# Kernel optimization log

Measured on AMD Instinct MI355X. Metric: run time of the kernel, lower is better.

The kernel has to match this reference:

```python
import jax, jax.numpy as jnp
import numpy as np

B, S, H, F, E, TOP_K = 2, 2048, 1024, 2048, 8, 2


def setup_inputs() -> dict:
    key = jax.random.key(0)
    ks = jax.random.split(key, 5)
    scale_h = 1.0 / np.sqrt(H)
    scale_f = 1.0 / np.sqrt(F)
    return {
        "hidden_states": jax.random.normal(ks[0], (B, S, H), jnp.float32),
        "gate_w": jax.random.normal(ks[1], (H, E), jnp.float32) * scale_h,
        "w_up": jax.random.normal(ks[2], (E, H, F), jnp.float32) * scale_h,
        "w_gate": jax.random.normal(ks[3], (E, H, F), jnp.float32) * scale_h,
        "w_down": jax.random.normal(ks[4], (E, F, H), jnp.float32) * scale_f,
    }


def reference(hidden_states, gate_w, w_up, w_gate, w_down):
    b, s, h = hidden_states.shape
    x = hidden_states.reshape(-1, h)                      # [T, H]
    T = x.shape[0]

    # Router: softmax then top-k then renormalize (as in the module)
    router_logits = x @ gate_w                            # [T, E]
    probs = jax.nn.softmax(router_logits, axis=-1)
    routing_weights, selected_experts = jax.lax.top_k(probs, TOP_K)  # [T, K]
    routing_weights = routing_weights / jnp.sum(routing_weights, axis=-1, keepdims=True)
    routing_weights = routing_weights.astype(x.dtype)

    # Per-token combine weight for each expert (sum over k where selected == e).
    # Equals the masked where/+ accumulation in the original (zero where unselected).
    combine = jnp.zeros((T, E), x.dtype).at[
        jnp.arange(T)[:, None], selected_experts
    ].add(routing_weights)                                # [T, E]

    # Dense expert compute on ALL tokens for every expert (faithful to original,
    # where each device runs its expert on the full token set, then psum).
    up = jnp.einsum("th,ehf->etf", x, w_up)               # [E, T, F]
    gate = jnp.einsum("th,ehf->etf", x, w_gate)           # [E, T, F]
    inner = jax.nn.silu(up) * gate                        # note: silu on up_proj, as in source
    expert_out = jnp.einsum("etf,efh->eth", inner, w_down)  # [E, T, H]

    # Weighted combine == psum over expert axis of masked/weighted outputs.
    y = jnp.einsum("te,eth->th", combine, expert_out)     # [T, H]
    return y.reshape(b, s, h)
```

## Files before the change

### kernel.cpp

```cpp
#include <hip/hip_runtime.h>
#include <hip/hip_bf16.h>

typedef __bf16 bf16x8 __attribute__((ext_vector_type(8)));
typedef float f32x4 __attribute__((ext_vector_type(4)));

#define T_TOK 4096
#define H_DIM 1024
#define F_DIM 2048
#define NEXP 8
#define TOTROWS 8192
#define MAXTILES 80

__device__ inline unsigned short f2b(float f) {
    unsigned int u = __float_as_uint(f);
    unsigned int r = (u + 0x7fffu + ((u >> 16) & 1u)) >> 16;
    return (unsigned short)r;
}

__global__ __launch_bounds__(256) void router_kernel(const float* __restrict__ x,
                                                     const float* __restrict__ gw,
                                                     int* __restrict__ sel, float* __restrict__ selw) {
    int t = blockIdx.x * 4 + (threadIdx.x >> 6);
    int lane = threadIdx.x & 63;
    float acc[8] = {0.f,0.f,0.f,0.f,0.f,0.f,0.f,0.f};
    const float* xr = x + (size_t)t * H_DIM;
    for (int h = lane; h < H_DIM; h += 64) {
        float xv = xr[h];
        const float4* g = (const float4*)(gw + h * 8);
        float4 g0 = g[0], g1 = g[1];
        acc[0] += xv * g0.x; acc[1] += xv * g0.y; acc[2] += xv * g0.z; acc[3] += xv * g0.w;
        acc[4] += xv * g1.x; acc[5] += xv * g1.y; acc[6] += xv * g1.z; acc[7] += xv * g1.w;
    }
#pragma unroll
    for (int off = 32; off >= 1; off >>= 1)
#pragma unroll
        for (int e = 0; e < 8; ++e)
            acc[e] += __shfl_down(acc[e], off);
    if (lane == 0) {
        float mx = acc[0];
#pragma unroll
        for (int e = 1; e < 8; ++e) mx = fmaxf(mx, acc[e]);
        float p[8]; float s = 0.f;
#pragma unroll
        for (int e = 0; e < 8; ++e) { p[e] = expf(acc[e] - mx); s += p[e]; }
        float inv_s = 1.f / s;
#pragma unroll
        for (int e = 0; e < 8; ++e) p[e] *= inv_s;
        int e1 = 0; float p1 = p[0];
#pragma unroll
        for (int e = 1; e < 8; ++e) if (p[e] > p1) { p1 = p[e]; e1 = e; }
        int e2 = -1; float p2 = -1.f;
#pragma unroll
        for (int e = 0; e < 8; ++e) { if (e == e1) continue; if (p[e] > p2) { p2 = p[e]; e2 = e; } }
        float inv = 1.f / (p1 + p2);
        sel[t * 2 + 0] = e1; sel[t * 2 + 1] = e2;
        selw[t * 2 + 0] = p1 * inv; selw[t * 2 + 1] = p2 * inv;
    }
}

__global__ __launch_bounds__(256) void scan_kernel(const int* __restrict__ sel,
                                                   int* __restrict__ cnt, int* __restrict__ off,
                                                   int* __restrict__ fill,
                                                   int* __restrict__ tileExp, int* __restrict__ tileM0) {
    __shared__ int h[NEXP];
    int tid = threadIdx.x;
    if (tid < NEXP) h[tid] = 0;
    __syncthreads();
    for (int i = tid; i < TOTROWS; i += 256) atomicAdd(&h[sel[i]], 1);
    __syncthreads();
    if (tid == 0) {
        int o = 0;
        for (int e = 0; e < NEXP; ++e) { cnt[e] = h[e]; off[e] = o; o += h[e]; fill[e] = 0; }
        int nt = 0;
        for (int e = 0; e < NEXP; ++e)
            for (int m0 = 0; m0 < h[e]; m0 += 128) { tileExp[nt] = e; tileM0[nt] = m0; nt++; }
        for (int i = nt; i < MAXTILES; ++i) { tileExp[i] = -1; tileM0[i] = 0; }
    }
}

__global__ __launch_bounds__(256) void scatgath_kernel(const int* __restrict__ sel,
                                                       const float* __restrict__ selw,
                                                       const int* __restrict__ off,
                                                       int* __restrict__ fill,
                                                       float* __restrict__ rowWgt,
                                                       int* __restrict__ tokRow,
                                                       const float* __restrict__ x,
                                                       unsigned short* __restrict__ Xg) {
    __shared__ int rs[2];
    int t = blockIdx.x;
    int tid = threadIdx.x;
    if (tid == 0) {
#pragma unroll
        for (int k = 0; k < 2; ++k) {
            int e = sel[t * 2 + k];
            int slot = atomicAdd(&fill[e], 1);
            int r = off[e] + slot;
            rowWgt[r] = selw[t * 2 + k];
            tokRow[t * 2 + k] = r;
            rs[k] = r;
        }
    }
    __syncthreads();
    int r1 = rs[0], r2 = rs[1];
    float4 v = ((const float4*)(x + (size_t)t * H_DIM))[tid];
    ushort4 o;
    o.x = f2b(v.x); o.y = f2b(v.y); o.z = f2b(v.z); o.w = f2b(v.w);
    ((ushort4*)(Xg + (size_t)r1 * H_DIM))[tid] = o;
    ((ushort4*)(Xg + (size_t)r2 * H_DIM))[tid] = o;
}

__global__ __launch_bounds__(256) void transpose_cvt_kernel(
        const float* __restrict__ w_up, const float* __restrict__ w_gate,
        const float* __restrict__ w_down,
        unsigned short* __restrict__ wTu, unsigned short* __restrict__ wTg,
        unsigned short* __restrict__ wTd) {
    __shared__ unsigned short lt[64 * 68];
    int z = blockIdx.z;
    int e = blockIdx.y;
    const float* src; unsigned short* dst; int R, C, tr, tc;
    if (z == 0)      { src = w_up;   dst = wTu; R = H_DIM; C = F_DIM; }
    else if (z == 1) { src = w_gate; dst = wTg; R = H_DIM; C = F_DIM; }
    else             { src = w_down; dst = wTd; R = F_DIM; C = H_DIM; }
    if (R == H_DIM) { tc = blockIdx.x & 31; tr = blockIdx.x >> 5; }
    else            { tc = blockIdx.x & 15; tr = blockIdx.x >> 4; }
    const float* s = src + (size_t)e * H_DIM * F_DIM;
    unsigned short* d = dst + (size_t)e * H_DIM * F_DIM;
    int r0 = tr * 64, c0 = tc * 64;
    int tid = threadIdx.x;
    int fc = tid & 15, row = tid >> 4;
#pragma unroll
    for (int i = 0; i < 4; ++i) {
        int r = row + i * 16;
        float4 v = *(const float4*)(s + (size_t)(r0 + r) * C + c0 + fc * 4);
        lt[(fc * 4 + 0) * 68 + r] = f2b(v.x);
        lt[(fc * 4 + 1) * 68 + r] = f2b(v.y);
        lt[(fc * 4 + 2) * 68 + r] = f2b(v.z);
        lt[(fc * 4 + 3) * 68 + r] = f2b(v.w);
    }
    __syncthreads();
    int ch = tid & 7, cc = tid >> 3;
#pragma unroll
    for (int i = 0; i < 2; ++i) {
        int c = cc + i * 32;
        uint2 lo = *(const uint2*)&lt[c * 68 + ch * 8];
        uint2 hi = *(const uint2*)&lt[c * 68 + ch * 8 + 4];
        uint4 o = make_uint4(lo.x, lo.y, hi.x, hi.y);
        *(uint4*)(d + (size_t)(c0 + c) * R + r0 + ch * 8) = o;
    }
}

__global__ __launch_bounds__(256, 2) void gemm_upgate_kernel(
        const unsigned short* __restrict__ Xg,
        const unsigned short* __restrict__ wTu,
        const unsigned short* __restrict__ wTg,
        unsigned short* __restrict__ inner,
        const int* __restrict__ tileExp, const int* __restrict__ tileM0,
        const int* __restrict__ off, const int* __restrict__ cnt) {
    __shared__ __align__(16) unsigned short la[2][4096];
    __shared__ __align__(16) unsigned short lbu[2][4096];
    __shared__ __align__(16) unsigned short lbg[2][4096];
    int bt = blockIdx.y;
    int e = tileExp[bt];
    if (e < 0) return;
    int m0 = tileM0[bt];
    int r0 = off[e] + m0;
    int valid = cnt[e] - m0;
    int f0 = blockIdx.x * 128;
    const unsigned short* aB  = Xg + (size_t)r0 * H_DIM;
    const unsigned short* buW = wTu + (size_t)e * F_DIM * H_DIM + (size_t)f0 * H_DIM;
    const unsigned short* bgW = wTg + (size_t)e * F_DIM * H_DIM + (size_t)f0 * H_DIM;
    int tid = threadIdx.x;
    int lane = tid & 63, wid = tid >> 6;
    int wm = wid >> 1, wn = wid & 1;
    int l16 = lane & 15, quad = lane >> 4;

    int rA0 = tid >> 2, rA1 = rA0 + 64;
    int s0 = rA0 * H_DIM + (tid & 3) * 8;
    int s1 = rA1 * H_DIM + (tid & 3) * 8;
    int d0 = rA0 * 32 + (((tid & 3) ^ (rA0 & 3)) << 3);
    int d1 = rA1 * 32 + (((tid & 3) ^ (rA1 & 3)) << 3);

    int aIdx[4], bIdx[4];
#pragma unroll
    for (int i = 0; i < 4; ++i) {
        int lr = wm * 64 + i * 16 + l16;
        aIdx[i] = lr * 32 + ((quad ^ (lr & 3)) << 3);
    }
#pragma unroll
    for (int j = 0; j < 4; ++j) {
        int lr = wn * 64 + j * 16 + l16;
        bIdx[j] = lr * 32 + ((quad ^ (lr & 3)) << 3);
    }

    f32x4 accU[4][4], accG[4][4];
#pragma unroll
    for (int i = 0; i < 4; ++i)
#pragma unroll
        for (int j = 0; j < 4; ++j) { accU[i][j] = (f32x4)0.f; accG[i][j] = (f32x4)0.f; }

    uint4 va0, va1, vu0, vu1, vg0, vg1;

#define UPG_LOAD(K0) do {                                        \
    va0 = *(const uint4*)(aB + s0 + (K0));                       \
    va1 = *(const uint4*)(aB + s1 + (K0));                       \
    vu0 = *(const uint4*)(buW + s0 + (K0));                      \
    vu1 = *(const uint4*)(buW + s1 + (K0));                      \
    vg0 = *(const uint4*)(bgW + s0 + (K0));                      \
    vg1 = *(const uint4*)(bgW + s1 + (K0));                      \
} while (0)
#define UPG_WRITE(NB) do {                                       \
    *(uint4*)&la[NB][d0]  = va0;  *(uint4*)&la[NB][d1]  = va1;   \
    *(uint4*)&lbu[NB][d0] = vu0;  *(uint4*)&lbu[NB][d1] = vu1;   \
    *(uint4*)&lbg[NB][d0] = vg0;  *(uint4*)&lbg[NB][d1] = vg1;   \
} while (0)

    UPG_LOAD(0);
    UPG_WRITE(0);
    UPG_LOAD(32);
    asm volatile("s_waitcnt lgkmcnt(0)" ::: "memory");
    __builtin_amdgcn_s_barrier();
    __builtin_amdgcn_sched_barrier(0);

    for (int t = 0; t < 32; ++t) {
        int cur = t & 1, nxt = cur ^ 1;
        const unsigned short* lac = la[cur];
        const unsigned short* luc = lbu[cur];
        const unsigned short* lgc = lbg[cur];
        bf16x8 af[4], bu[4], bg[4];
#pragma unroll
        for (int i = 0; i < 4; ++i) af[i] = *(const bf16x8*)(lac + aIdx[i]);
#pragma unroll
        for (int j = 0; j < 4; ++j) {
            bu[j] = *(const bf16x8*)(luc + bIdx[j]);
            bg[j] = *(const bf16x8*)(lgc + bIdx[j]);
        }
        if (t < 31) UPG_WRITE(nxt);
        if (t < 30) UPG_LOAD((t + 2) * 32);
        __builtin_amdgcn_s_setprio(1);
#pragma unroll
        for (int i = 0; i < 4; ++i)
#pragma unroll
            for (int j = 0; j < 4; ++j) {
                accU[i][j] = __builtin_amdgcn_mfma_f32_16x16x32_bf16(af[i], bu[j], accU[i][j], 0, 0, 0);
                accG[i][j] = __builtin_amdgcn_mfma_f32_16x16x32_bf16(af[i], bg[j], accG[i][j], 0, 0, 0);
            }
        __builtin_amdgcn_s_setprio(0);
        asm volatile("s_waitcnt lgkmcnt(0)" ::: "memory");
        __builtin_amdgcn_s_barrier();
        __builtin_amdgcn_sched_barrier(0);
    }
#undef UPG_LOAD
#undef UPG_WRITE

#pragma unroll
    for (int i = 0; i < 4; ++i) {
#pragma unroll
        for (int rr = 0; rr < 4; ++rr) {
            int ml = wm * 64 + i * 16 + quad * 4 + rr;
            if (ml >= valid) continue;
            size_t base = (size_t)(r0 + ml) * F_DIM + f0;
#pragma unroll
            for (int j = 0; j < 4; ++j) {
                float u = accU[i][j][rr];
                float g = accG[i][j][rr];
                float v = u * __builtin_amdgcn_rcpf(1.f + __expf(-u)) * g;
                inner[base + wn * 64 + j * 16 + l16] = f2b(v);
            }
        }
    }
}

__global__ __launch_bounds__(256, 3) void gemm_down_kernel(
        const unsigned short* __restrict__ inner,
        const unsigned short* __restrict__ wTd,
        float* __restrict__ part,
        const int* __restrict__ tileExp, const int* __restrict__ tileM0,
        const int* __restrict__ off, const int* __restrict__ cnt,
        const float* __restrict__ rowWgt) {
    __shared__ __align__(16) unsigned short la[2][4096];
    __shared__ __align__(16) unsigned short lb[2][4096];
    int bt = blockIdx.y;
    int e = tileExp[bt];
    if (e < 0) return;
    int m0 = tileM0[bt];
    int r0 = off[e] + m0;
    int valid = cnt[e] - m0;
    int h0 = blockIdx.x * 128;
    const unsigned short* aB = inner + (size_t)r0 * F_DIM;
    const unsigned short* bp = wTd + (size_t)e * H_DIM * F_DIM + (size_t)h0 * F_DIM;
    int tid = threadIdx.x;
    int lane = tid & 63, wid = tid >> 6;
    int wm = wid >> 1, wn = wid & 1;
    int l16 = lane & 15, quad = lane >> 4;

    int rA0 = tid >> 2, rA1 = rA0 + 64;
    int s0 = rA0 * F_DIM + (tid & 3) * 8;
    int s1 = rA1 * F_DIM + (tid & 3) * 8;
    int d0 = rA0 * 32 + (((tid & 3) ^ (rA0 & 3)) << 3);
    int d1 = rA1 * 32 + (((tid & 3) ^ (rA1 & 3)) << 3);

    int aIdx[4], bIdx[4];
#pragma unroll
    for (int i = 0; i < 4; ++i) {
        int lr = wm * 64 + i * 16 + l16;
        aIdx[i] = lr * 32 + ((quad ^ (lr & 3)) << 3);
    }
#pragma unroll
    for (int j = 0; j < 4; ++j) {
        int lr = wn * 64 + j * 16 + l16;
        bIdx[j] = lr * 32 + ((quad ^ (lr & 3)) << 3);
    }

    f32x4 acc[4][4];
#pragma unroll
    for (int i = 0; i < 4; ++i)
#pragma unroll
        for (int j = 0; j < 4; ++j) acc[i][j] = (f32x4)0.f;

    uint4 va0, va1, vb0, vb1;

#define DWN_LOAD(K0) do {                                        \
    va0 = *(const uint4*)(aB + s0 + (K0));                       \
    va1 = *(const uint4*)(aB + s1 + (K0));                       \
    vb0 = *(const uint4*)(bp + s0 + (K0));                       \
    vb1 = *(const uint4*)(bp + s1 + (K0));                       \
} while (0)
#define DWN_WRITE(NB) do {                                       \
    *(uint4*)&la[NB][d0] = va0;  *(uint4*)&la[NB][d1] = va1;     \
    *(uint4*)&lb[NB][d0] = vb0;  *(uint4*)&lb[NB][d1] = vb1;     \
} while (0)

    DWN_LOAD(0);
    DWN_WRITE(0);
    DWN_LOAD(32);
    asm volatile("s_waitcnt lgkmcnt(0)" ::: "memory");
    __builtin_amdgcn_s_barrier();
    __builtin_amdgcn_sched_barrier(0);

    for (int t = 0; t < 64; ++t) {
        int cur = t & 1, nxt = cur ^ 1;
        const unsigned short* lac = la[cur];
        const unsigned short* lbc = lb[cur];
        bf16x8 af[4], bw[4];
#pragma unroll
        for (int i = 0; i < 4; ++i) af[i] = *(const bf16x8*)(lac + aIdx[i]);
#pragma unroll
        for (int j = 0; j < 4; ++j) bw[j] = *(const bf16x8*)(lbc + bIdx[j]);
        if (t < 63) DWN_WRITE(nxt);
        if (t < 62) DWN_LOAD((t + 2) * 32);
        __builtin_amdgcn_s_setprio(1);
#pragma unroll
        for (int i = 0; i < 4; ++i)
#pragma unroll
            for (int j = 0; j < 4; ++j)
                acc[i][j] = __builtin_amdgcn_mfma_f32_16x16x32_bf16(af[i], bw[j], acc[i][j], 0, 0, 0);
        __builtin_amdgcn_s_setprio(0);
        asm volatile("s_waitcnt lgkmcnt(0)" ::: "memory");
        __builtin_amdgcn_s_barrier();
        __builtin_amdgcn_sched_barrier(0);
    }
#undef DWN_LOAD
#undef DWN_WRITE

#pragma unroll
    for (int i = 0; i < 4; ++i) {
#pragma unroll
        for (int rr = 0; rr < 4; ++rr) {
            int ml = wm * 64 + i * 16 + quad * 4 + rr;
            if (ml >= valid) continue;
            int gr = r0 + ml;
            float w = rowWgt[gr];
            float* orow = part + (size_t)gr * H_DIM + h0;
#pragma unroll
            for (int j = 0; j < 4; ++j)
                orow[wn * 64 + j * 16 + l16] = w * acc[i][j][rr];
        }
    }
}

__global__ __launch_bounds__(256) void combine_kernel(const float* __restrict__ part,
                                                      const int* __restrict__ tokRow,
                                                      float* __restrict__ out) {
    int t = blockIdx.x;
    int r1 = tokRow[t * 2 + 0], r2 = tokRow[t * 2 + 1];
    int i = threadIdx.x;
    float4 a = ((const float4*)(part + (size_t)r1 * H_DIM))[i];
    float4 b = ((const float4*)(part + (size_t)r2 * H_DIM))[i];
    float4 o;
    o.x = a.x + b.x; o.y = a.y + b.y; o.z = a.z + b.z; o.w = a.w + b.w;
    ((float4*)(out + (size_t)t * H_DIM))[i] = o;
}

extern "C" void kernel_launch(void* const* d_in, const int* in_sizes, int n_in,
                              void* d_out, int out_size, void* d_ws, size_t ws_size,
                              hipStream_t stream) {
    const float* x      = (const float*)d_in[0];
    const float* gw     = (const float*)d_in[1];
    const float* w_up   = (const float*)d_in[2];
    const float* w_gate = (const float*)d_in[3];
    const float* w_down = (const float*)d_in[4];
    float* out = (float*)d_out;

    char* ws = (char*)d_ws;
    size_t o = 0;
    unsigned short* wTu = (unsigned short*)(ws + o); o += (size_t)NEXP * F_DIM * H_DIM * 2;
    unsigned short* wTg = (unsigned short*)(ws + o); o += (size_t)NEXP * F_DIM * H_DIM * 2;
    unsigned short* wTd = (unsigned short*)(ws + o); o += (size_t)NEXP * H_DIM * F_DIM * 2;
    unsigned short* Xg  = (unsigned short*)(ws + o); o += (size_t)TOTROWS * H_DIM * 2;
    unsigned short* inner = (unsigned short*)(ws + o); o += (size_t)TOTROWS * F_DIM * 2;
    o += 2 * 1024 * 1024;
    float* rowWgt = (float*)(ws + o); o += TOTROWS * 4;
    int*   tokRow = (int*)(ws + o);   o += T_TOK * 2 * 4;
    int*   sel    = (int*)(ws + o);   o += T_TOK * 2 * 4;
    float* selw   = (float*)(ws + o); o += T_TOK * 2 * 4;
    int*   cnt    = (int*)(ws + o);   o += 8 * 4;
    int*   fill   = (int*)(ws + o);   o += 8 * 4;
    int*   off_   = (int*)(ws + o);   o += 8 * 4;
    int*   tileExp = (int*)(ws + o);  o += MAXTILES * 4;
    int*   tileM0  = (int*)(ws + o);  o += MAXTILES * 4;
    float* part = (float*)wTu;

    router_kernel<<<T_TOK / 4, 256, 0, stream>>>(x, gw, sel, selw);
    scan_kernel<<<1, 256, 0, stream>>>(sel, cnt, off_, fill, tileExp, tileM0);
    scatgath_kernel<<<T_TOK, 256, 0, stream>>>(sel, selw, off_, fill, rowWgt, tokRow, x, Xg);
    transpose_cvt_kernel<<<dim3(512, NEXP, 3), 256, 0, stream>>>(w_up, w_gate, w_down, wTu, wTg, wTd);
    gemm_upgate_kernel<<<dim3(F_DIM / 128, 72), 256, 0, stream>>>(Xg, wTu, wTg, inner, tileExp, tileM0, off_, cnt);
    gemm_down_kernel<<<dim3(H_DIM / 128, 72), 256, 0, stream>>>(inner, wTd, part, tileExp, tileM0, off_, cnt, rowWgt);
    combine_kernel<<<T_TOK, 256, 0, stream>>>(part, tokRow, out);
}
```

Measured before the change: 502.0 us.

## Load A fragments directly from global in up/gate GEMM; batch row assignment

The up/gate GEMM drops the LDS staging buffer for the activation tile. Each wave now loads its A fragments straight from global memory into registers, double-buffered one step ahead, with the loop unrolled by two to alternate register sets. This cuts LDS traffic and footprint, but each A element is now read from global/L2 by both column waves instead of once. Separately, the per-token atomic slot assignment becomes a ballot/popcount assign kernel that does one atomic per expert per block, followed by a plain copy kernel, at the cost of one extra launch.

Result: faster. 446.7 us (-11.0%).

```diff
diff --git a/kernel.cpp b/kernel.cpp
--- a/kernel.cpp
+++ b/kernel.cpp
@@ -78,30 +78,44 @@
     }
 }
 
-__global__ __launch_bounds__(256) void scatgath_kernel(const int* __restrict__ sel,
-                                                       const float* __restrict__ selw,
-                                                       const int* __restrict__ off,
-                                                       int* __restrict__ fill,
-                                                       float* __restrict__ rowWgt,
-                                                       int* __restrict__ tokRow,
-                                                       const float* __restrict__ x,
-                                                       unsigned short* __restrict__ Xg) {
-    __shared__ int rs[2];
+__global__ __launch_bounds__(256) void assign_kernel(const int* __restrict__ sel,
+                                                     const float* __restrict__ selw,
+                                                     const int* __restrict__ off,
+                                                     int* __restrict__ fill,
+                                                     float* __restrict__ rowWgt,
+                                                     int* __restrict__ tokRow) {
+    __shared__ int wcnt[4][NEXP];
+    __shared__ int bbase[NEXP];
+    int tid = threadIdx.x, lane = tid & 63, w = tid >> 6;
+    int i = blockIdx.x * 256 + tid;
+    int e = sel[i];
+    unsigned long long below = (1ULL << lane) - 1;
+    int myrank = 0;
+#pragma unroll
+    for (int x = 0; x < NEXP; ++x) {
+        unsigned long long m = __ballot(e == x);
+        if (lane == 0) wcnt[w][x] = __popcll(m);
+        if (e == x) myrank = __popcll(m & below);
+    }
+    __syncthreads();
+    if (tid < NEXP) {
+        int tot = wcnt[0][tid] + wcnt[1][tid] + wcnt[2][tid] + wcnt[3][tid];
+        bbase[tid] = atomicAdd(&fill[tid], tot);
+    }
+    __syncthreads();
+    int wb = 0;
+    for (int w2 = 0; w2 < w; ++w2) wb += wcnt[w2][e];
+    int r = off[e] + bbase[e] + wb + myrank;
+    tokRow[i] = r;
+    rowWgt[r] = selw[i];
+}
+
+__global__ __launch_bounds__(256) void copy_kernel(const int* __restrict__ tokRow,
+                                                   const float* __restrict__ x,
+                                                   unsigned short* __restrict__ Xg) {
     int t = blockIdx.x;
     int tid = threadIdx.x;
-    if (tid == 0) {
-#pragma unroll
-        for (int k = 0; k < 2; ++k) {
-            int e = sel[t * 2 + k];
-            int slot = atomicAdd(&fill[e], 1);
-            int r = off[e] + slot;
-            rowWgt[r] = selw[t * 2 + k];
-            tokRow[t * 2 + k] = r;
-            rs[k] = r;
-        }
-    }
-    __syncthreads();
-    int r1 = rs[0], r2 = rs[1];
+    int r1 = tokRow[t * 2 + 0], r2 = tokRow[t * 2 + 1];
     float4 v = ((const float4*)(x + (size_t)t * H_DIM))[tid];
     ushort4 o;
     o.x = f2b(v.x); o.y = f2b(v.y); o.z = f2b(v.z); o.w = f2b(v.w);
@@ -156,7 +170,6 @@
         unsigned short* __restrict__ inner,
         const int* __restrict__ tileExp, const int* __restrict__ tileM0,
         const int* __restrict__ off, const int* __restrict__ cnt) {
-    __shared__ __align__(16) unsigned short la[2][4096];
     __shared__ __align__(16) unsigned short lbu[2][4096];
     __shared__ __align__(16) unsigned short lbg[2][4096];
     int bt = blockIdx.y;
@@ -174,23 +187,23 @@
     int wm = wid >> 1, wn = wid & 1;
     int l16 = lane & 15, quad = lane >> 4;
 
-    int rA0 = tid >> 2, rA1 = rA0 + 64;
-    int s0 = rA0 * H_DIM + (tid & 3) * 8;
-    int s1 = rA1 * H_DIM + (tid & 3) * 8;
-    int d0 = rA0 * 32 + (((tid & 3) ^ (rA0 & 3)) << 3);
-    int d1 = rA1 * 32 + (((tid & 3) ^ (rA1 & 3)) << 3);
-
-    int aIdx[4], bIdx[4];
-#pragma unroll
-    for (int i = 0; i < 4; ++i) {
-        int lr = wm * 64 + i * 16 + l16;
-        aIdx[i] = lr * 32 + ((quad ^ (lr & 3)) << 3);
-    }
+    int rB0 = tid >> 2, rB1 = rB0 + 64;
+    int s0 = rB0 * H_DIM + (tid & 3) * 8;
+    int s1 = rB1 * H_DIM + (tid & 3) * 8;
+    int d0 = rB0 * 32 + (((tid & 3) ^ (rB0 & 3)) << 3);
+    int d1 = rB1 * 32 + (((tid & 3) ^ (rB1 & 3)) << 3);
+
+    int bIdx[4], aOff[4];
 #pragma unroll
     for (int j = 0; j < 4; ++j) {
         int lr = wn * 64 + j * 16 + l16;
         bIdx[j] = lr * 32 + ((quad ^ (lr & 3)) << 3);
     }
+#pragma unroll
+    for (int i = 0; i < 4; ++i) {
+        int lr = wm * 64 + i * 16 + l16;
+        aOff[i] = lr * H_DIM + quad * 8;
+    }
 
     f32x4 accU[4][4], accG[4][4];
 #pragma unroll
@@ -198,59 +211,61 @@
 #pragma unroll
         for (int j = 0; j < 4; ++j) { accU[i][j] = (f32x4)0.f; accG[i][j] = (f32x4)0.f; }
 
-    uint4 va0, va1, vu0, vu1, vg0, vg1;
-
-#define UPG_LOAD(K0) do {                                        \
-    va0 = *(const uint4*)(aB + s0 + (K0));                       \
-    va1 = *(const uint4*)(aB + s1 + (K0));                       \
+    bf16x8 afA[4], afB[4];
+    uint4 vu0, vu1, vg0, vg1;
+
+#define UPG_BLOAD(K0) do {                                       \
     vu0 = *(const uint4*)(buW + s0 + (K0));                      \
     vu1 = *(const uint4*)(buW + s1 + (K0));                      \
     vg0 = *(const uint4*)(bgW + s0 + (K0));                      \
     vg1 = *(const uint4*)(bgW + s1 + (K0));                      \
 } while (0)
-#define UPG_WRITE(NB) do {                                       \
-    *(uint4*)&la[NB][d0]  = va0;  *(uint4*)&la[NB][d1]  = va1;   \
+#define UPG_BWRITE(NB) do {                                      \
     *(uint4*)&lbu[NB][d0] = vu0;  *(uint4*)&lbu[NB][d1] = vu1;   \
     *(uint4*)&lbg[NB][d0] = vg0;  *(uint4*)&lbg[NB][d1] = vg1;   \
 } while (0)
-
-    UPG_LOAD(0);
-    UPG_WRITE(0);
-    UPG_LOAD(32);
+#define UPG_ALOAD(AF, K0) do {                                   \
+    _Pragma("unroll") for (int i_ = 0; i_ < 4; ++i_)             \
+        AF[i_] = *(const bf16x8*)(aB + aOff[i_] + (K0));         \
+} while (0)
+
+    UPG_ALOAD(afA, 0);
+    UPG_BLOAD(0);
+    UPG_BWRITE(0);
+    UPG_BLOAD(32);
     asm volatile("s_waitcnt lgkmcnt(0)" ::: "memory");
     __builtin_amdgcn_s_barrier();
     __builtin_amdgcn_sched_barrier(0);
 
-    for (int t = 0; t < 32; ++t) {
-        int cur = t & 1, nxt = cur ^ 1;
-        const unsigned short* lac = la[cur];
-        const unsigned short* luc = lbu[cur];
-        const unsigned short* lgc = lbg[cur];
-        bf16x8 af[4], bu[4], bg[4];
-#pragma unroll
-        for (int i = 0; i < 4; ++i) af[i] = *(const bf16x8*)(lac + aIdx[i]);
-#pragma unroll
-        for (int j = 0; j < 4; ++j) {
-            bu[j] = *(const bf16x8*)(luc + bIdx[j]);
-            bg[j] = *(const bf16x8*)(lgc + bIdx[j]);
-        }
-        if (t < 31) UPG_WRITE(nxt);
-        if (t < 30) UPG_LOAD((t + 2) * 32);
-        __builtin_amdgcn_s_setprio(1);
-#pragma unroll
-        for (int i = 0; i < 4; ++i)
-#pragma unroll
-            for (int j = 0; j < 4; ++j) {
-                accU[i][j] = __builtin_amdgcn_mfma_f32_16x16x32_bf16(af[i], bu[j], accU[i][j], 0, 0, 0);
-                accG[i][j] = __builtin_amdgcn_mfma_f32_16x16x32_bf16(af[i], bg[j], accG[i][j], 0, 0, 0);
-            }
-        __builtin_amdgcn_s_setprio(0);
-        asm volatile("s_waitcnt lgkmcnt(0)" ::: "memory");
-        __builtin_amdgcn_s_barrier();
-        __builtin_amdgcn_sched_barrier(0);
-    }
-#undef UPG_LOAD
-#undef UPG_WRITE
+#define UPG_STEP(T, CUR, NXT, AFC, AFN) do {                                      \
+    bf16x8 bu_[4], bg_[4];                                                        \
+    _Pragma("unroll") for (int j_ = 0; j_ < 4; ++j_) {                            \
+        bu_[j_] = *(const bf16x8*)&lbu[CUR][bIdx[j_]];                            \
+        bg_[j_] = *(const bf16x8*)&lbg[CUR][bIdx[j_]];                            \
+    }                                                                             \
+    if ((T) < 31) UPG_BWRITE(NXT);                                                \
+    if ((T) < 31) UPG_ALOAD(AFN, ((T) + 1) * 32);                                 \
+    if ((T) < 30) UPG_BLOAD(((T) + 2) * 32);                                      \
+    __builtin_amdgcn_s_setprio(1);                                                \
+    _Pragma("unroll") for (int i_ = 0; i_ < 4; ++i_)                              \
+        _Pragma("unroll") for (int j_ = 0; j_ < 4; ++j_) {                        \
+            accU[i_][j_] = __builtin_amdgcn_mfma_f32_16x16x32_bf16(AFC[i_], bu_[j_], accU[i_][j_], 0, 0, 0); \
+            accG[i_][j_] = __builtin_amdgcn_mfma_f32_16x16x32_bf16(AFC[i_], bg_[j_], accG[i_][j_], 0, 0, 0); \
+        }                                                                         \
+    __builtin_amdgcn_s_setprio(0);                                                \
+    asm volatile("s_waitcnt lgkmcnt(0)" ::: "memory");                            \
+    __builtin_amdgcn_s_barrier();                                                 \
+    __builtin_amdgcn_sched_barrier(0);                                            \
+} while (0)
+
+    for (int t = 0; t < 32; t += 2) {
+        UPG_STEP(t,     0, 1, afA, afB);
+        UPG_STEP(t + 1, 1, 0, afB, afA);
+    }
+#undef UPG_STEP
+#undef UPG_ALOAD
+#undef UPG_BLOAD
+#undef UPG_BWRITE
 
 #pragma unroll
     for (int i = 0; i < 4; ++i) {
@@ -422,7 +437,8 @@
 
     router_kernel<<<T_TOK / 4, 256, 0, stream>>>(x, gw, sel, selw);
     scan_kernel<<<1, 256, 0, stream>>>(sel, cnt, off_, fill, tileExp, tileM0);
-    scatgath_kernel<<<T_TOK, 256, 0, stream>>>(sel, selw, off_, fill, rowWgt, tokRow, x, Xg);
+    assign_kernel<<<TOTROWS / 256, 256, 0, stream>>>(sel, selw, off_, fill, rowWgt, tokRow);
+    copy_kernel<<<T_TOK, 256, 0, stream>>>(tokRow, x, Xg);
     transpose_cvt_kernel<<<dim3(512, NEXP, 3), 256, 0, stream>>>(w_up, w_gate, w_down, wTu, wTg, wTd);
     gemm_upgate_kernel<<<dim3(F_DIM / 128, 72), 256, 0, stream>>>(Xg, wTu, wTg, inner, tileExp, tileM0, off_, cnt);
     gemm_down_kernel<<<dim3(H_DIM / 128, 72), 256, 0, stream>>>(inner, wTd, part, tileExp, tileM0, off_, cnt, rowWgt);
```
